# Optimization experiments

Measured on AMD Instinct MI355X. Metric: run time of the kernel, lower is better.

The kernel has to match this reference:

```python
import jax, jax.numpy as jnp
import numpy as np

B, IC, OC, OUT_DIM, S = 64, 128, 128, 1024, 2
L = OUT_DIM * S  # 2048


def setup_inputs() -> dict:
    key = jax.random.key(0)
    k1, k2 = jax.random.split(key)
    x = jax.random.normal(k1, (B, IC, L), dtype=jnp.float32)
    weight = jax.random.normal(k2, (OC, IC, L), dtype=jnp.float32)
    return {"x": x, "weight": weight}


def reference(x, weight):
    # Faithful to: (x[:,None]*weight).view(B,OC,IC,-1,2).sum(dims=[-1,-3]) / sqrt(IC)
    # Fused as a single contraction over input_channels and the size-2 patch axis,
    # never materializing the (B,OC,IC,L) intermediate.
    ic = x.shape[1]
    xr = x.reshape(x.shape[0], ic, -1, 2)          # (B, IC, out_dim, 2)
    wr = weight.reshape(weight.shape[0], ic, -1, 2)  # (OC, IC, out_dim, 2)
    out = jnp.einsum('bids,oids->bod', xr, wr)       # (B, OC, out_dim)
    return out / jnp.sqrt(jnp.asarray(ic, dtype=x.dtype))
```

## Files before the change

kernel.cpp:

```cpp
#include <hip/hip_runtime.h>

#define B_SZ   64
#define IC_N   128
#define OC_N   128
#define OUT_D  1024
#define L_N    2048

#define D_TILE 8
#define N_TILE 32
#define KC     16
#define KPAD   40

typedef __attribute__((ext_vector_type(8))) __bf16          bf16x8;
typedef __attribute__((ext_vector_type(8))) unsigned short  u16x8;
typedef __attribute__((ext_vector_type(4))) float           f32x4;

__device__ __forceinline__ unsigned pack2bf(float lo, float hi) {
    unsigned ul = __builtin_bit_cast(unsigned, lo);
    unsigned uh = __builtin_bit_cast(unsigned, hi);
    ul += 0x7fffu + ((ul >> 16) & 1u);
    uh += 0x7fffu + ((uh >> 16) & 1u);
    return (ul >> 16) | (uh & 0xffff0000u);
}

__global__ __launch_bounds__(256, 2)
void lc1d_kernel(const float* __restrict__ x, const float* __restrict__ w,
                 float* __restrict__ out) {
    __shared__ __align__(16) unsigned short Xs[D_TILE][B_SZ][KPAD];
    __shared__ __align__(16) unsigned short Ws[D_TILE][N_TILE][KPAD];

    const int t     = threadIdx.x;
    const int wv_id = t >> 6;
    const int lane  = t & 63;
    const int col   = lane & 15;
    const int quad  = lane >> 4;

    const int oc_blk = blockIdx.x & 3;
    const int dg     = blockIdx.x >> 2;
    const int o0     = oc_blk * N_TILE;
    const int l0     = dg * (2 * D_TILE);

    f32x4 acc[2][4][2];
#pragma unroll
    for (int dl = 0; dl < 2; ++dl)
#pragma unroll
        for (int mt = 0; mt < 4; ++mt)
#pragma unroll
            for (int nt = 0; nt < 2; ++nt)
                acc[dl][mt][nt] = (f32x4){0.f, 0.f, 0.f, 0.f};

    for (int chunk = 0; chunk < IC_N / KC; ++chunk) {
        const int i0 = chunk * KC;

        float4 xv[16];
#pragma unroll
        for (int r = 0; r < 16; ++r) {
            const int f  = t + 256 * r;
            const int b  = f >> 6;
            const int il = (f >> 2) & 15;
            const int j  = f & 3;
            xv[r] = *(const float4*)&x[(size_t)(b * IC_N + i0 + il) * L_N + l0 + 4 * j];
        }
        float4 wvv[8];
#pragma unroll
        for (int r = 0; r < 8; ++r) {
            const int f  = t + 256 * r;
            const int ol = f >> 6;
            const int il = (f >> 2) & 15;
            const int j  = f & 3;
            wvv[r] = *(const float4*)&w[(size_t)((o0 + ol) * IC_N + i0 + il) * L_N + l0 + 4 * j];
        }

        __syncthreads();

#pragma unroll
        for (int r = 0; r < 16; ++r) {
            const int f  = t + 256 * r;
            const int b  = f >> 6;
            const int il = (f >> 2) & 15;
            const int j  = f & 3;
            *(unsigned*)&Xs[2 * j][b][2 * il]     = pack2bf(xv[r].x, xv[r].y);
            *(unsigned*)&Xs[2 * j + 1][b][2 * il] = pack2bf(xv[r].z, xv[r].w);
        }
#pragma unroll
        for (int r = 0; r < 8; ++r) {
            const int f  = t + 256 * r;
            const int ol = f >> 6;
            const int il = (f >> 2) & 15;
            const int j  = f & 3;
            *(unsigned*)&Ws[2 * j][ol][2 * il]     = pack2bf(wvv[r].x, wvv[r].y);
            *(unsigned*)&Ws[2 * j + 1][ol][2 * il] = pack2bf(wvv[r].z, wvv[r].w);
        }

        __syncthreads();

#pragma unroll
        for (int dl = 0; dl < 2; ++dl) {
            const int dp = 2 * wv_id + dl;
            bf16x8 afr[4];
            bf16x8 bfr[2];
#pragma unroll
            for (int mt = 0; mt < 4; ++mt)
                afr[mt] = __builtin_bit_cast(bf16x8,
                    *(const u16x8*)&Xs[dp][16 * mt + col][quad * 8]);
#pragma unroll
            for (int nt = 0; nt < 2; ++nt)
                bfr[nt] = __builtin_bit_cast(bf16x8,
                    *(const u16x8*)&Ws[dp][16 * nt + col][quad * 8]);
#pragma unroll
            for (int mt = 0; mt < 4; ++mt)
#pragma unroll
                for (int nt = 0; nt < 2; ++nt)
                    acc[dl][mt][nt] = __builtin_amdgcn_mfma_f32_16x16x32_bf16(
                        afr[mt], bfr[nt], acc[dl][mt][nt], 0, 0, 0);
        }
    }

    const float scale = 0.088388347648318447f;
    const int dbase = dg * D_TILE + 2 * wv_id;
#pragma unroll
    for (int mt = 0; mt < 4; ++mt)
#pragma unroll
        for (int nt = 0; nt < 2; ++nt)
#pragma unroll
            for (int reg = 0; reg < 4; ++reg) {
                const int b = 16 * mt + 4 * quad + reg;
                const int o = o0 + 16 * nt + col;
                float2 v;
                v.x = acc[0][mt][nt][reg] * scale;
                v.y = acc[1][mt][nt][reg] * scale;
                *(float2*)&out[(size_t)(b * OC_N + o) * OUT_D + dbase] = v;
            }
}

extern "C" void kernel_launch(void* const* d_in, const int* in_sizes, int n_in,
                              void* d_out, int out_size, void* d_ws, size_t ws_size,
                              hipStream_t stream) {
    const float* x = (const float*)d_in[0];
    const float* w = (const float*)d_in[1];
    float* out     = (float*)d_out;

    dim3 grid(512);
    dim3 block(256);
    hipLaunchKernelGGL(lc1d_kernel, grid, block, 0, stream, x, w, out);
}
```

Baseline: 329.0 us.

## Split into bf16 repack pass and fragment-layout MFMA GEMM kernel

Adds a repack kernel that converts x and weight to bf16 and writes them straight into the MFMA fragment order in workspace. A second kernel then loads those fragments directly from global memory with no LDS staging or barriers. The goal is to remove strided fp32 gathers and shared-memory transposes from the GEMM. In exchange it adds an extra kernel launch and a full write and re-read of bf16 copies of both inputs. The old kernel remains as a fallback for when the workspace is too small.

```diff
diff --git a/kernel.cpp b/kernel.cpp
--- a/kernel.cpp
+++ b/kernel.cpp
@@ -5,11 +5,6 @@
 #define OC_N   128
 #define OUT_D  1024
 #define L_N    2048
-
-#define D_TILE 8
-#define N_TILE 32
-#define KC     16
-#define KPAD   40
 
 typedef __attribute__((ext_vector_type(8))) __bf16          bf16x8;
 typedef __attribute__((ext_vector_type(8))) unsigned short  u16x8;
@@ -23,9 +18,124 @@
     return (ul >> 16) | (uh & 0xffff0000u);
 }
 
+__global__ __launch_bounds__(256, 4)
+void repack_kernel(const float* __restrict__ x, const float* __restrict__ w,
+                   unsigned short* __restrict__ xf, unsigned short* __restrict__ wf) {
+    __shared__ unsigned tile[16 * 16 * 33];
+
+    const int bid = blockIdx.x;
+    const int t    = threadIdx.x;
+    const int ic_l = t & 15;
+    const int r_l  = t >> 4;
+    const int wv   = t >> 6, lane = t & 63;
+    const int col  = lane & 15, quad = lane >> 4;
+
+    const bool isw = (bid >= 256);
+    int dg, ch, rg;
+    if (!isw) { dg = bid & 7;  ch = (bid >> 3) & 7;  rg = bid >> 6; }
+    else      { const int b2 = bid - 256; dg = b2 & 7; ch = (b2 >> 3) & 7; rg = b2 >> 6; }
+
+    const float* src = isw ? w : x;
+    const float* srow = src + (size_t)((rg * 16 + r_l) * 128 + ch * 16 + ic_l) * L_N + dg * 256;
+
+    for (int p = 0; p < 4; ++p) {
+        float4 v[16];
+#pragma unroll
+        for (int k = 0; k < 16; ++k)
+            v[k] = *(const float4*)&srow[p * 64 + 4 * k];
+
+        __syncthreads();
+
+#pragma unroll
+        for (int k = 0; k < 16; ++k) {
+            const int base = (ic_l * 16 + r_l) * 33 + 2 * k;
+            tile[base]     = pack2bf(v[k].x, v[k].y);
+            tile[base + 1] = pack2bf(v[k].z, v[k].w);
+        }
+
+        __syncthreads();
+
+#pragma unroll
+        for (int dd = 0; dd < 8; ++dd) {
+            const int dl = wv * 8 + dd;
+            unsigned dw0 = tile[((4 * quad + 0) * 16 + col) * 33 + dl];
+            unsigned dw1 = tile[((4 * quad + 1) * 16 + col) * 33 + dl];
+            unsigned dw2 = tile[((4 * quad + 2) * 16 + col) * 33 + dl];
+            unsigned dw3 = tile[((4 * quad + 3) * 16 + col) * 33 + dl];
+            const int d = dg * 128 + p * 32 + dl;
+            size_t slot;
+            unsigned short* dst;
+            if (!isw) {
+                slot = (((size_t)d * 8 + ch) * 4 + rg) * 64 + lane;
+                dst = xf;
+            } else {
+                slot = ((((size_t)(rg >> 1) * 1024 + d) * 8 + ch) * 2 + (rg & 1)) * 64 + lane;
+                dst = wf;
+            }
+            *(uint4*)&dst[slot * 8] = make_uint4(dw0, dw1, dw2, dw3);
+        }
+    }
+}
+
+__global__ __launch_bounds__(256, 4)
+void gemm_frag_kernel(const unsigned short* __restrict__ xf,
+                      const unsigned short* __restrict__ wf,
+                      float* __restrict__ out) {
+    const int bid = blockIdx.x;
+    const int ocb = bid & 3;
+    const int dm  = bid >> 2;
+    const int t   = threadIdx.x, wv = t >> 6, lane = t & 63;
+    const int col = lane & 15, quad = lane >> 4;
+    const int d   = dm * 4 + wv;
+
+    const u16x8* xp = (const u16x8*)xf + (size_t)d * 2048 + lane;
+    const u16x8* wp = (const u16x8*)wf + ((size_t)ocb * 1024 + d) * 1024 + lane;
+
+    f32x4 acc[4][2];
+#pragma unroll
+    for (int mt = 0; mt < 4; ++mt)
+#pragma unroll
+        for (int nt = 0; nt < 2; ++nt)
+            acc[mt][nt] = (f32x4){0.f, 0.f, 0.f, 0.f};
+
+#pragma unroll
+    for (int ch = 0; ch < 8; ++ch) {
+        bf16x8 a[4], b[2];
+#pragma unroll
+        for (int mt = 0; mt < 4; ++mt)
+            a[mt] = __builtin_bit_cast(bf16x8, xp[ch * 256 + mt * 64]);
+#pragma unroll
+        for (int nt = 0; nt < 2; ++nt)
+            b[nt] = __builtin_bit_cast(bf16x8, wp[ch * 128 + nt * 64]);
+#pragma unroll
+        for (int mt = 0; mt < 4; ++mt)
+#pragma unroll
+            for (int nt = 0; nt < 2; ++nt)
+                acc[mt][nt] = __builtin_amdgcn_mfma_f32_16x16x32_bf16(
+                    a[mt], b[nt], acc[mt][nt], 0, 0, 0);
+    }
+
+    const float scale = 0.088388347648318447f;
+#pragma unroll
+    for (int mt = 0; mt < 4; ++mt)
+#pragma unroll
+        for (int nt = 0; nt < 2; ++nt)
+#pragma unroll
+            for (int r = 0; r < 4; ++r) {
+                const int b = 16 * mt + 4 * quad + r;
+                const int o = 32 * ocb + 16 * nt + col;
+                out[(size_t)(b * OC_N + o) * OUT_D + d] = acc[mt][nt][r] * scale;
+            }
+}
+
+#define D_TILE 8
+#define N_TILE 32
+#define KC     16
+#define KPAD   40
+
 __global__ __launch_bounds__(256, 2)
-void lc1d_kernel(const float* __restrict__ x, const float* __restrict__ w,
-                 float* __restrict__ out) {
+void lc1d_fallback(const float* __restrict__ x, const float* __restrict__ w,
+                   float* __restrict__ out) {
     __shared__ __align__(16) unsigned short Xs[D_TILE][B_SZ][KPAD];
     __shared__ __align__(16) unsigned short Ws[D_TILE][N_TILE][KPAD];
 
@@ -51,49 +161,32 @@
 
     for (int chunk = 0; chunk < IC_N / KC; ++chunk) {
         const int i0 = chunk * KC;
-
         float4 xv[16];
 #pragma unroll
         for (int r = 0; r < 16; ++r) {
-            const int f  = t + 256 * r;
-            const int b  = f >> 6;
-            const int il = (f >> 2) & 15;
-            const int j  = f & 3;
+            const int f = t + 256 * r, b = f >> 6, il = (f >> 2) & 15, j = f & 3;
             xv[r] = *(const float4*)&x[(size_t)(b * IC_N + i0 + il) * L_N + l0 + 4 * j];
         }
         float4 wvv[8];
 #pragma unroll
         for (int r = 0; r < 8; ++r) {
-            const int f  = t + 256 * r;
-            const int ol = f >> 6;
-            const int il = (f >> 2) & 15;
-            const int j  = f & 3;
+            const int f = t + 256 * r, ol = f >> 6, il = (f >> 2) & 15, j = f & 3;
             wvv[r] = *(const float4*)&w[(size_t)((o0 + ol) * IC_N + i0 + il) * L_N + l0 + 4 * j];
         }
-
-        __syncthreads();
-
+        __syncthreads();
 #pragma unroll
         for (int r = 0; r < 16; ++r) {
-            const int f  = t + 256 * r;
-            const int b  = f >> 6;
-            const int il = (f >> 2) & 15;
-            const int j  = f & 3;
+            const int f = t + 256 * r, b = f >> 6, il = (f >> 2) & 15, j = f & 3;
             *(unsigned*)&Xs[2 * j][b][2 * il]     = pack2bf(xv[r].x, xv[r].y);
             *(unsigned*)&Xs[2 * j + 1][b][2 * il] = pack2bf(xv[r].z, xv[r].w);
         }
 #pragma unroll
         for (int r = 0; r < 8; ++r) {
-            const int f  = t + 256 * r;
-            const int ol = f >> 6;
-            const int il = (f >> 2) & 15;
-            const int j  = f & 3;
+            const int f = t + 256 * r, ol = f >> 6, il = (f >> 2) & 15, j = f & 3;
             *(unsigned*)&Ws[2 * j][ol][2 * il]     = pack2bf(wvv[r].x, wvv[r].y);
             *(unsigned*)&Ws[2 * j + 1][ol][2 * il] = pack2bf(wvv[r].z, wvv[r].w);
         }
-
-        __syncthreads();
-
+        __syncthreads();
 #pragma unroll
         for (int dl = 0; dl < 2; ++dl) {
             const int dp = 2 * wv_id + dl;
@@ -101,12 +194,10 @@
             bf16x8 bfr[2];
 #pragma unroll
             for (int mt = 0; mt < 4; ++mt)
-                afr[mt] = __builtin_bit_cast(bf16x8,
-                    *(const u16x8*)&Xs[dp][16 * mt + col][quad * 8]);
+                afr[mt] = __builtin_bit_cast(bf16x8, *(const u16x8*)&Xs[dp][16 * mt + col][quad * 8]);
 #pragma unroll
             for (int nt = 0; nt < 2; ++nt)
-                bfr[nt] = __builtin_bit_cast(bf16x8,
-                    *(const u16x8*)&Ws[dp][16 * nt + col][quad * 8]);
+                bfr[nt] = __builtin_bit_cast(bf16x8, *(const u16x8*)&Ws[dp][16 * nt + col][quad * 8]);
 #pragma unroll
             for (int mt = 0; mt < 4; ++mt)
 #pragma unroll
@@ -126,10 +217,10 @@
             for (int reg = 0; reg < 4; ++reg) {
                 const int b = 16 * mt + 4 * quad + reg;
                 const int o = o0 + 16 * nt + col;
-                float2 v;
-                v.x = acc[0][mt][nt][reg] * scale;
-                v.y = acc[1][mt][nt][reg] * scale;
-                *(float2*)&out[(size_t)(b * OC_N + o) * OUT_D + dbase] = v;
+                float2 v2;
+                v2.x = acc[0][mt][nt][reg] * scale;
+                v2.y = acc[1][mt][nt][reg] * scale;
+                *(float2*)&out[(size_t)(b * OC_N + o) * OUT_D + dbase] = v2;
             }
 }
 
@@ -140,7 +231,15 @@
     const float* w = (const float*)d_in[1];
     float* out     = (float*)d_out;
 
-    dim3 grid(512);
-    dim3 block(256);
-    hipLaunchKernelGGL(lc1d_kernel, grid, block, 0, stream, x, w, out);
-}
+    const size_t XF_BYTES = (size_t)B_SZ * IC_N * L_N * 2;
+    const size_t WF_BYTES = (size_t)OC_N * IC_N * L_N * 2;
+
+    if (ws_size >= XF_BYTES + WF_BYTES) {
+        unsigned short* xf = (unsigned short*)d_ws;
+        unsigned short* wfp = (unsigned short*)((char*)d_ws + XF_BYTES);
+        hipLaunchKernelGGL(repack_kernel, dim3(768), dim3(256), 0, stream, x, w, xf, wfp);
+        hipLaunchKernelGGL(gemm_frag_kernel, dim3(1024), dim3(256), 0, stream, xf, wfp, out);
+    } else {
+        hipLaunchKernelGGL(lc1d_fallback, dim3(512), dim3(256), 0, stream, x, w, out);
+    }
+}
```

New measurement: 368.3 us. +11.9%, slower.
